# Optimization experiments

Hardware: AMD Instinct MI355X
Metric: run time of the kernel (lower is better)

The kernel has to match this reference:

```python
import jax, jax.numpy as jnp
import numpy as np

B, L, CZ, CH = 1, 512, 128, 128
LN_EPS = 1e-5  # torch nn.LayerNorm default


def layer_norm(x, g, b, eps=LN_EPS):
    mu = jnp.mean(x, axis=-1, keepdims=True)
    var = jnp.var(x, axis=-1, keepdims=True)
    return (x - mu) * jax.lax.rsqrt(var + eps) * g + b


def setup_inputs() -> dict:
    key = jax.random.key(0)
    ks = jax.random.split(key, 16)
    def lin(k, fan_in, fan_out):
        bound = 1.0 / np.sqrt(fan_in)
        kw, kb = jax.random.split(k)
        W = jax.random.uniform(kw, (fan_out, fan_in), jnp.float32, -bound, bound)
        b = jax.random.uniform(kb, (fan_out,), jnp.float32, -bound, bound)
        return W, b
    z = jax.random.normal(ks[0], (B, L, L, CZ), jnp.float32)
    pair_mask = jnp.ones((B, L, L), jnp.float32)
    Wap, bap = lin(ks[1], CZ, CH)
    Wbp, bbp = lin(ks[2], CZ, CH)
    Wag, bag = lin(ks[3], CZ, CH)
    Wbg, bbg = lin(ks[4], CZ, CH)
    Wo, bo = lin(ks[5], CH, CZ)
    Wg, bg = lin(ks[6], CZ, CZ)
    return {
        "z": z, "pair_mask": pair_mask,
        "ln_in_g": jnp.ones((CZ,), jnp.float32), "ln_in_b": jnp.zeros((CZ,), jnp.float32),
        "Wap": Wap, "bap": bap, "Wbp": Wbp, "bbp": bbp,
        "Wag": Wag, "bag": bag, "Wbg": Wbg, "bbg": bbg,
        "ln_out_g": jnp.ones((CH,), jnp.float32), "ln_out_b": jnp.zeros((CH,), jnp.float32),
        "Wo": Wo, "bo": bo, "Wg": Wg, "bg": bg,
    }


def reference(z, pair_mask, ln_in_g, ln_in_b, Wap, bap, Wbp, bbp, Wag, bag,
              Wbg, bbg, ln_out_g, ln_out_b, Wo, bo, Wg, bg):
    # z: [B,L,L,c_z], pair_mask: [B,L,L]
    z_norm = layer_norm(z, ln_in_g, ln_in_b)
    a = (z_norm @ Wap.T + bap) * jax.nn.sigmoid(z_norm @ Wag.T + bag)  # [B,L,L,ch]
    b = (z_norm @ Wbp.T + bbp) * jax.nn.sigmoid(z_norm @ Wbg.T + bbg)
    m = pair_mask[..., None]
    a = a * m
    b = b * m
    # outgoing triangle contraction: c_hidden batched LxL matmuls
    x = jnp.einsum('bikc,bjkc->bijc', a, b)
    valid_k = jnp.einsum('bik,bjk->bij', pair_mask, pair_mask)
    x = x / jnp.sqrt(jnp.maximum(valid_k[..., None], 1.0))
    x = layer_norm(x, ln_out_g, ln_out_b)
    x = x @ Wo.T + bo
    gate = jax.nn.sigmoid(z_norm @ Wg.T + bg)
    x = x * gate  # dropout is identity in eval mode
    x = x * m
    return x
```

## Files before the change

kernel.cpp:

```cpp
#include <hip/hip_runtime.h>
#include <stdint.h>

typedef unsigned short u16;
typedef __bf16 bf16x8 __attribute__((ext_vector_type(8)));
typedef float  f32x4 __attribute__((ext_vector_type(4)));
typedef u16    u16x8 __attribute__((ext_vector_type(8)));
typedef u16    u16x4 __attribute__((ext_vector_type(4)));

constexpr int LL = 512;
constexpr int NROW = LL * LL;

__device__ __forceinline__ u16 f2b(float f) {
    union { float f; unsigned u; } v; v.f = f;
    return (u16)((v.u + 0x7fffu + ((v.u >> 16) & 1u)) >> 16);
}
__device__ __forceinline__ float b2f(u16 s) {
    union { unsigned u; float f; } v; v.u = ((unsigned)s) << 16; return v.f;
}
__device__ __forceinline__ float sigmoidf_(float x) { return 1.0f / (1.0f + __expf(-x)); }

__device__ __forceinline__ f32x4 mfma16(bf16x8 a, bf16x8 b, f32x4 c) {
    return __builtin_amdgcn_mfma_f32_16x16x32_bf16(a, b, c, 0, 0, 0);
}

__global__ __launch_bounds__(256)
void k0_wconv(const float* __restrict__ Wap, const float* __restrict__ Wag,
              const float* __restrict__ Wbp, const float* __restrict__ Wbg,
              const float* __restrict__ Wg, const float* __restrict__ Wo,
              u16* __restrict__ wbf)
{
    const float* srcs[6] = {Wap, Wag, Wbp, Wbg, Wg, Wo};
    const int m = blockIdx.x >> 6;
    const int e = ((blockIdx.x & 63) << 8) | threadIdx.x;
    wbf[m * 16384 + e] = f2b(srcs[m][e]);
}

__global__ __launch_bounds__(256, 2)
void k1_ln_proj(const float* __restrict__ z, const float* __restrict__ mask,
                const float* __restrict__ lg, const float* __restrict__ lb,
                const u16* __restrict__ Wapb, const float* __restrict__ bap,
                const u16* __restrict__ Wagb, const float* __restrict__ bag,
                const u16* __restrict__ Wbpb, const float* __restrict__ bbp,
                const u16* __restrict__ Wbgb, const float* __restrict__ bbg,
                const u16* __restrict__ Wgb, const float* __restrict__ bgv,
                u16* __restrict__ a_t, u16* __restrict__ b_t, float* __restrict__ gate)
{
    __shared__ __align__(16) u16 Zs[128][136];
    __shared__ float Gg[128], Gb[128], Ms[128];

    const int tid = threadIdx.x;
    const int row0 = blockIdx.x * 128;

    if (tid < 128) { Gg[tid] = lg[tid]; Gb[tid] = lb[tid]; Ms[tid] = mask[row0 + tid]; }

    const int r = tid >> 1, h = (tid & 1) * 64;
    const float* zrow = z + (size_t)(row0 + r) * 128 + h;
    float s1 = 0.f, s2 = 0.f;
#pragma unroll
    for (int j = 0; j < 64; j += 4) {
        f32x4 v = *(const f32x4*)(zrow + j);
#pragma unroll
        for (int e = 0; e < 4; ++e) { s1 += v[e]; s2 += v[e] * v[e]; }
    }
    s1 += __shfl_xor(s1, 1);
    s2 += __shfl_xor(s2, 1);
    const float mu = s1 * 0.0078125f;
    const float rs = rsqrtf(fmaxf(s2 * 0.0078125f - mu * mu, 0.f) + 1e-5f);
    __syncthreads();
#pragma unroll
    for (int j = 0; j < 64; j += 4) {
        f32x4 v = *(const f32x4*)(zrow + j);
        u16x4 o;
#pragma unroll
        for (int e = 0; e < 4; ++e)
            o[e] = f2b((v[e] - mu) * rs * Gg[h + j + e] + Gb[h + j + e]);
        *(u16x4*)&Zs[r][h + j] = o;
    }
    __syncthreads();

    const int lane = tid & 63, wave = tid >> 6;
    const int wm = (wave >> 1) * 64, wn = (wave & 1) * 64;
    const int lr = lane & 15, quad = lane >> 4, kq = quad * 8;

#pragma unroll 1
    for (int pair = 0; pair < 2; ++pair) {
        const u16* WP = pair ? Wbpb : Wapb;
        const float* BP = pair ? bbp : bap;
        const u16* WG = pair ? Wbgb : Wagb;
        const float* BG = pair ? bbg : bag;
        u16* outp = pair ? b_t : a_t;

        f32x4 accP[4][4], accG[4][4];
#pragma unroll
        for (int i = 0; i < 4; ++i)
#pragma unroll
            for (int j = 0; j < 4; ++j) {
                accP[i][j] = (f32x4){0.f, 0.f, 0.f, 0.f};
                accG[i][j] = (f32x4){0.f, 0.f, 0.f, 0.f};
            }
#pragma unroll
        for (int kk = 0; kk < 128; kk += 32) {
            bf16x8 af[4];
#pragma unroll
            for (int mt = 0; mt < 4; ++mt)
                af[mt] = *(const bf16x8*)&Zs[wm + mt * 16 + lr][kk + kq];
#pragma unroll
            for (int nt = 0; nt < 4; ++nt) {
                const int ncol = wn + nt * 16 + lr;
                bf16x8 bp8 = *(const bf16x8*)(WP + ncol * 128 + kk + kq);
                bf16x8 bg8 = *(const bf16x8*)(WG + ncol * 128 + kk + kq);
#pragma unroll
                for (int mt = 0; mt < 4; ++mt) {
                    accP[mt][nt] = mfma16(af[mt], bp8, accP[mt][nt]);
                    accG[mt][nt] = mfma16(af[mt], bg8, accG[mt][nt]);
                }
            }
        }
#pragma unroll
        for (int nt = 0; nt < 4; ++nt) {
            const int ncol = wn + nt * 16 + lr;
            const float bP = BP[ncol];
            const float bG = BG[ncol];
#pragma unroll
            for (int mt = 0; mt < 4; ++mt) {
                const int rb = wm + mt * 16 + quad * 4;
                u16x4 o;
#pragma unroll
                for (int e = 0; e < 4; ++e)
                    o[e] = f2b((accP[mt][nt][e] + bP) * sigmoidf_(accG[mt][nt][e] + bG) * Ms[rb + e]);
                *(u16x4*)(outp + (size_t)ncol * NROW + row0 + rb) = o;
            }
        }
    }

    {
        f32x4 acc[4][4];
#pragma unroll
        for (int i = 0; i < 4; ++i)
#pragma unroll
            for (int j = 0; j < 4; ++j) acc[i][j] = (f32x4){0.f, 0.f, 0.f, 0.f};
#pragma unroll
        for (int kk = 0; kk < 128; kk += 32) {
            bf16x8 af[4];
#pragma unroll
            for (int mt = 0; mt < 4; ++mt)
                af[mt] = *(const bf16x8*)&Zs[wm + mt * 16 + lr][kk + kq];
#pragma unroll
            for (int nt = 0; nt < 4; ++nt) {
                bf16x8 bw = *(const bf16x8*)(Wgb + (wn + nt * 16 + lr) * 128 + kk + kq);
#pragma unroll
                for (int mt = 0; mt < 4; ++mt) acc[mt][nt] = mfma16(af[mt], bw, acc[mt][nt]);
            }
        }
#pragma unroll
        for (int nt = 0; nt < 4; ++nt) {
            const int ncol = wn + nt * 16 + lr;
            const float bb = bgv[ncol];
#pragma unroll
            for (int mt = 0; mt < 4; ++mt) {
                const int rb = wm + mt * 16 + quad * 4;
#pragma unroll
                for (int e = 0; e < 4; ++e)
                    gate[(size_t)(row0 + rb + e) * 128 + ncol] = sigmoidf_(acc[mt][nt][e] + bb);
            }
        }
    }
}

__global__ __launch_bounds__(256, 2)
void k2_scale(const float* __restrict__ mask, float* __restrict__ scale)
{
    __shared__ __align__(16) u16 As[128][72];
    __shared__ __align__(16) u16 Bs[128][72];

    const int tid = threadIdx.x;
    const int i0 = (blockIdx.x >> 2) * 128, j0 = (blockIdx.x & 3) * 128;
    const int lane = tid & 63, wave = tid >> 6;
    const int wm = (wave >> 1) * 64, wn = (wave & 1) * 64;
    const int lr = lane & 15, quad = lane >> 4, kq = quad * 8;

    f32x4 acc[4][4];
#pragma unroll
    for (int i = 0; i < 4; ++i)
#pragma unroll
        for (int j = 0; j < 4; ++j) acc[i][j] = (f32x4){0.f, 0.f, 0.f, 0.f};

    for (int kc = 0; kc < LL; kc += 64) {
#pragma unroll
        for (int p = 0; p < 8; ++p) {
            const int q = p * 256 + tid, rr = q >> 4, ko = (q & 15) * 4;
            f32x4 va = *(const f32x4*)(mask + (size_t)(i0 + rr) * LL + kc + ko);
            f32x4 vb = *(const f32x4*)(mask + (size_t)(j0 + rr) * LL + kc + ko);
            u16x4 ca, cb;
#pragma unroll
            for (int e = 0; e < 4; ++e) { ca[e] = f2b(va[e]); cb[e] = f2b(vb[e]); }
            *(u16x4*)&As[rr][ko] = ca;
            *(u16x4*)&Bs[rr][ko] = cb;
        }
        __syncthreads();
#pragma unroll
        for (int kk = 0; kk < 64; kk += 32) {
            bf16x8 af[4], bf[4];
#pragma unroll
            for (int mt = 0; mt < 4; ++mt) af[mt] = *(const bf16x8*)&As[wm + mt * 16 + lr][kk + kq];
#pragma unroll
            for (int nt = 0; nt < 4; ++nt) bf[nt] = *(const bf16x8*)&Bs[wn + nt * 16 + lr][kk + kq];
#pragma unroll
            for (int mt = 0; mt < 4; ++mt)
#pragma unroll
                for (int nt = 0; nt < 4; ++nt) acc[mt][nt] = mfma16(af[mt], bf[nt], acc[mt][nt]);
        }
        __syncthreads();
    }
#pragma unroll
    for (int mt = 0; mt < 4; ++mt)
#pragma unroll
        for (int nt = 0; nt < 4; ++nt) {
            const int gj = j0 + wn + nt * 16 + lr;
#pragma unroll
            for (int e = 0; e < 4; ++e) {
                const int gi = i0 + wm + mt * 16 + quad * 4 + e;
                scale[(size_t)gi * LL + gj] = rsqrtf(fmaxf(acc[mt][nt][e], 1.0f));
            }
        }
}

__global__ __launch_bounds__(256, 2)
void k3_einsum(const u16* __restrict__ a_t, const u16* __restrict__ b_t,
               const float* __restrict__ scale, u16* __restrict__ x_t)
{
    __shared__ __align__(16) u16 pool[2 * 128 * 72];
    u16 (*As)[72] = (u16(*)[72])pool;
    u16 (*Bs)[72] = (u16(*)[72])(pool + 128 * 72);
    u16 (*Ss)[128] = (u16(*)[128])pool;

    const int bid = blockIdx.x;
    const int xcd = bid & 7, slot = bid >> 3;
    const int c = xcd * 16 + (slot >> 4);
    const int tile = slot & 15;
    const int i0 = (tile >> 2) * 128, j0 = (tile & 3) * 128;

    const u16* A = a_t + (size_t)c * NROW;
    const u16* B = b_t + (size_t)c * NROW;

    const int tid = threadIdx.x;
    const int lane = tid & 63, wave = tid >> 6;
    const int wm = (wave >> 1) * 64, wn = (wave & 1) * 64;
    const int lr = lane & 15, quad = lane >> 4, kq = quad * 8;

    f32x4 acc[4][4];
#pragma unroll
    for (int i = 0; i < 4; ++i)
#pragma unroll
        for (int j = 0; j < 4; ++j) acc[i][j] = (f32x4){0.f, 0.f, 0.f, 0.f};

    for (int kc = 0; kc < LL; kc += 64) {
#pragma unroll
        for (int p = 0; p < 4; ++p) {
            const int q = p * 256 + tid, rr = q >> 3, ko = (q & 7) * 8;
            *(u16x8*)&As[rr][ko] = *(const u16x8*)(A + (size_t)(i0 + rr) * LL + kc + ko);
            *(u16x8*)&Bs[rr][ko] = *(const u16x8*)(B + (size_t)(j0 + rr) * LL + kc + ko);
        }
        __syncthreads();
#pragma unroll
        for (int kk = 0; kk < 64; kk += 32) {
            bf16x8 af[4], bf[4];
#pragma unroll
            for (int mt = 0; mt < 4; ++mt) af[mt] = *(const bf16x8*)&As[wm + mt * 16 + lr][kk + kq];
#pragma unroll
            for (int nt = 0; nt < 4; ++nt) bf[nt] = *(const bf16x8*)&Bs[wn + nt * 16 + lr][kk + kq];
#pragma unroll
            for (int mt = 0; mt < 4; ++mt)
#pragma unroll
                for (int nt = 0; nt < 4; ++nt) acc[mt][nt] = mfma16(af[mt], bf[nt], acc[mt][nt]);
        }
        __syncthreads();
    }
#pragma unroll
    for (int mt = 0; mt < 4; ++mt)
#pragma unroll
        for (int nt = 0; nt < 4; ++nt) {
            const int cc = wn + nt * 16 + lr;
#pragma unroll
            for (int e = 0; e < 4; ++e) {
                const int rr = wm + mt * 16 + quad * 4 + e;
                const float s = scale[(size_t)(i0 + rr) * LL + j0 + cc];
                Ss[rr][cc] = f2b(acc[mt][nt][e] * s);
            }
        }
    __syncthreads();
#pragma unroll
    for (int p = 0; p < 8; ++p) {
        const int rr = p * 16 + (tid >> 4);
        const int jo = (tid & 15) * 8;
        *(u16x8*)(x_t + (size_t)c * NROW + (size_t)(i0 + rr) * LL + j0 + jo) = *(const u16x8*)&Ss[rr][jo];
    }
}

__global__ __launch_bounds__(256, 2)
void k4_out(const u16* __restrict__ x_t, const float* __restrict__ mask,
            const float* __restrict__ lg, const float* __restrict__ lb,
            const u16* __restrict__ Wob, const float* __restrict__ bo,
            const float* gate, float* out)
{
    __shared__ __align__(16) u16 Zs[128][136];
    __shared__ float Ms[128];

    const int tid = threadIdx.x;
    const int row0 = blockIdx.x * 128;

    if (tid < 128) Ms[tid] = mask[row0 + tid];

    {
        const int ijo = (tid & 31) * 4;
        const int cb = (tid >> 5) * 4;
#pragma unroll
        for (int p = 0; p < 4; ++p) {
            const int c = p * 32 + cb;
            u16x4 v0 = *(const u16x4*)(x_t + (size_t)(c + 0) * NROW + row0 + ijo);
            u16x4 v1 = *(const u16x4*)(x_t + (size_t)(c + 1) * NROW + row0 + ijo);
            u16x4 v2 = *(const u16x4*)(x_t + (size_t)(c + 2) * NROW + row0 + ijo);
            u16x4 v3 = *(const u16x4*)(x_t + (size_t)(c + 3) * NROW + row0 + ijo);
#pragma unroll
            for (int i = 0; i < 4; ++i) {
                u16x4 w = { v0[i], v1[i], v2[i], v3[i] };
                *(u16x4*)&Zs[ijo + i][c] = w;
            }
        }
    }
    __syncthreads();

    {
        const int r = tid >> 1, h = (tid & 1) * 64;
        float s1 = 0.f, s2 = 0.f;
#pragma unroll
        for (int j = 0; j < 64; j += 8) {
            u16x8 v = *(const u16x8*)&Zs[r][h + j];
#pragma unroll
            for (int e = 0; e < 8; ++e) { float x = b2f(v[e]); s1 += x; s2 += x * x; }
        }
        s1 += __shfl_xor(s1, 1);
        s2 += __shfl_xor(s2, 1);
        const float mu = s1 * 0.0078125f;
        const float rs = rsqrtf(fmaxf(s2 * 0.0078125f - mu * mu, 0.f) + 1e-5f);
#pragma unroll
        for (int j = 0; j < 64; j += 8) {
            const int c = h + j;
            u16x8 v = *(const u16x8*)&Zs[r][c];
            u16x8 o;
#pragma unroll
            for (int e = 0; e < 8; ++e)
                o[e] = f2b((b2f(v[e]) - mu) * rs * lg[c + e] + lb[c + e]);
            *(u16x8*)&Zs[r][c] = o;
        }
    }
    __syncthreads();

    const int lane = tid & 63, wave = tid >> 6;
    const int wm = (wave >> 1) * 64, wn = (wave & 1) * 64;
    const int lr = lane & 15, quad = lane >> 4, kq = quad * 8;

    f32x4 acc[4][4];
#pragma unroll
    for (int i = 0; i < 4; ++i)
#pragma unroll
        for (int j = 0; j < 4; ++j) acc[i][j] = (f32x4){0.f, 0.f, 0.f, 0.f};

#pragma unroll
    for (int kk = 0; kk < 128; kk += 32) {
        bf16x8 af[4];
#pragma unroll
        for (int mt = 0; mt < 4; ++mt)
            af[mt] = *(const bf16x8*)&Zs[wm + mt * 16 + lr][kk + kq];
#pragma unroll
        for (int nt = 0; nt < 4; ++nt) {
            bf16x8 bw = *(const bf16x8*)(Wob + (wn + nt * 16 + lr) * 128 + kk + kq);
#pragma unroll
            for (int mt = 0; mt < 4; ++mt) acc[mt][nt] = mfma16(af[mt], bw, acc[mt][nt]);
        }
    }
#pragma unroll
    for (int nt = 0; nt < 4; ++nt) {
        const int cc = wn + nt * 16 + lr;
        const float bb = bo[cc];
#pragma unroll
        for (int mt = 0; mt < 4; ++mt) {
            const int rb = wm + mt * 16 + quad * 4;
#pragma unroll
            for (int e = 0; e < 4; ++e) {
                const size_t idx = (size_t)(row0 + rb + e) * 128 + cc;
                const float g = gate[idx];
                out[idx] = (acc[mt][nt][e] + bb) * g * Ms[rb + e];
            }
        }
    }
}

extern "C" void kernel_launch(void* const* d_in, const int* in_sizes, int n_in,
                              void* d_out, int out_size, void* d_ws, size_t ws_size,
                              hipStream_t stream)
{
    const float* z        = (const float*)d_in[0];
    const float* mask     = (const float*)d_in[1];
    const float* ln_in_g  = (const float*)d_in[2];
    const float* ln_in_b  = (const float*)d_in[3];
    const float* Wap      = (const float*)d_in[4];
    const float* bap      = (const float*)d_in[5];
    const float* Wbp      = (const float*)d_in[6];
    const float* bbp      = (const float*)d_in[7];
    const float* Wag      = (const float*)d_in[8];
    const float* bag      = (const float*)d_in[9];
    const float* Wbg      = (const float*)d_in[10];
    const float* bbg      = (const float*)d_in[11];
    const float* ln_out_g = (const float*)d_in[12];
    const float* ln_out_b = (const float*)d_in[13];
    const float* Wo       = (const float*)d_in[14];
    const float* bo       = (const float*)d_in[15];
    const float* Wg       = (const float*)d_in[16];
    const float* bg       = (const float*)d_in[17];

    u16* a_t = (u16*)d_ws;
    u16* b_t = a_t + (size_t)128 * NROW;
    u16* x_t = b_t + (size_t)128 * NROW;
    u16* wbf = x_t + (size_t)128 * NROW;
    float* scale = (float*)(wbf + 6 * 16384);
    float* gate = (float*)d_out;
    float* out  = (float*)d_out;

    const u16* Wapb = wbf + 0 * 16384;
    const u16* Wagb = wbf + 1 * 16384;
    const u16* Wbpb = wbf + 2 * 16384;
    const u16* Wbgb = wbf + 3 * 16384;
    const u16* Wgb  = wbf + 4 * 16384;
    const u16* Wob  = wbf + 5 * 16384;

    k0_wconv<<<dim3(384), dim3(256), 0, stream>>>(Wap, Wag, Wbp, Wbg, Wg, Wo, wbf);
    k1_ln_proj<<<dim3(2048), dim3(256), 0, stream>>>(z, mask, ln_in_g, ln_in_b,
        Wapb, bap, Wagb, bag, Wbpb, bbp, Wbgb, bbg, Wgb, bg, a_t, b_t, gate);
    k2_scale<<<dim3(16), dim3(256), 0, stream>>>(mask, scale);
    k3_einsum<<<dim3(2048), dim3(256), 0, stream>>>(a_t, b_t, scale, x_t);
    k4_out<<<dim3(2048), dim3(256), 0, stream>>>(x_t, mask, ln_out_g, ln_out_b, Wob, bo, gate, out);
}
```

Baseline: 659.1 us.

## Move gate projection to output kernel, merge scale kernel into projection launch

The gate GEMM moves out of the projection kernel and into the output kernel. The projection kernel now stores normalized z as bf16 into the output buffer, and the output kernel reads it back and computes sigmoid(zn·Wg) alongside the Wo GEMM. This replaces a 128MB fp32 gate write and read with a 64MB bf16 staging round trip. The mask-count scale computation is folded into the projection launch as 16 extra blocks, removing one kernel launch. The output kernel now holds two LDS tiles, which may lower occupancy, and f2b switches to the native bf16 conversion.

```diff
diff --git a/kernel.cpp b/kernel.cpp
--- a/kernel.cpp
+++ b/kernel.cpp
@@ -11,8 +11,8 @@
 constexpr int NROW = LL * LL;
 
 __device__ __forceinline__ u16 f2b(float f) {
-    union { float f; unsigned u; } v; v.f = f;
-    return (u16)((v.u + 0x7fffu + ((v.u >> 16) & 1u)) >> 16);
+    __bf16 h = (__bf16)f;
+    return __builtin_bit_cast(u16, h);
 }
 __device__ __forceinline__ float b2f(u16 s) {
     union { unsigned u; float f; } v; v.u = ((unsigned)s) << 16; return v.f;
@@ -42,14 +42,75 @@
                 const u16* __restrict__ Wagb, const float* __restrict__ bag,
                 const u16* __restrict__ Wbpb, const float* __restrict__ bbp,
                 const u16* __restrict__ Wbgb, const float* __restrict__ bbg,
-                const u16* __restrict__ Wgb, const float* __restrict__ bgv,
-                u16* __restrict__ a_t, u16* __restrict__ b_t, float* __restrict__ gate)
+                u16* __restrict__ a_t, u16* __restrict__ b_t,
+                float* __restrict__ scale, float* zn_out)
 {
-    __shared__ __align__(16) u16 Zs[128][136];
-    __shared__ float Gg[128], Gb[128], Ms[128];
+    __shared__ __align__(16) u16 pool[18432];
 
     const int tid = threadIdx.x;
-    const int row0 = blockIdx.x * 128;
+    const int lane = tid & 63, wave = tid >> 6;
+    const int wm = (wave >> 1) * 64, wn = (wave & 1) * 64;
+    const int lr = lane & 15, quad = lane >> 4, kq = quad * 8;
+
+    if (blockIdx.x < 16) {
+        u16 (*As)[72] = (u16(*)[72])pool;
+        u16 (*Bs)[72] = (u16(*)[72])(pool + 128 * 72);
+        const int sb = blockIdx.x;
+        const int i0 = (sb >> 2) * 128, j0 = (sb & 3) * 128;
+
+        f32x4 acc[4][4];
+#pragma unroll
+        for (int i = 0; i < 4; ++i)
+#pragma unroll
+            for (int j = 0; j < 4; ++j) acc[i][j] = (f32x4){0.f, 0.f, 0.f, 0.f};
+
+        for (int kc = 0; kc < LL; kc += 64) {
+#pragma unroll
+            for (int p = 0; p < 8; ++p) {
+                const int q = p * 256 + tid, rr = q >> 4, ko = (q & 15) * 4;
+                f32x4 va = *(const f32x4*)(mask + (size_t)(i0 + rr) * LL + kc + ko);
+                f32x4 vb = *(const f32x4*)(mask + (size_t)(j0 + rr) * LL + kc + ko);
+                u16x4 ca, cb;
+#pragma unroll
+                for (int e = 0; e < 4; ++e) { ca[e] = f2b(va[e]); cb[e] = f2b(vb[e]); }
+                *(u16x4*)&As[rr][ko] = ca;
+                *(u16x4*)&Bs[rr][ko] = cb;
+            }
+            __syncthreads();
+#pragma unroll
+            for (int kk = 0; kk < 64; kk += 32) {
+                bf16x8 af[4], bf[4];
+#pragma unroll
+                for (int mt = 0; mt < 4; ++mt) af[mt] = *(const bf16x8*)&As[wm + mt * 16 + lr][kk + kq];
+#pragma unroll
+                for (int nt = 0; nt < 4; ++nt) bf[nt] = *(const bf16x8*)&Bs[wn + nt * 16 + lr][kk + kq];
+#pragma unroll
+                for (int mt = 0; mt < 4; ++mt)
+#pragma unroll
+                    for (int nt = 0; nt < 4; ++nt) acc[mt][nt] = mfma16(af[mt], bf[nt], acc[mt][nt]);
+            }
+            __syncthreads();
+        }
+#pragma unroll
+        for (int mt = 0; mt < 4; ++mt)
+#pragma unroll
+            for (int nt = 0; nt < 4; ++nt) {
+                const int gj = j0 + wn + nt * 16 + lr;
+#pragma unroll
+                for (int e = 0; e < 4; ++e) {
+                    const int gi = i0 + wm + mt * 16 + quad * 4 + e;
+                    scale[(size_t)gi * LL + gj] = rsqrtf(fmaxf(acc[mt][nt][e], 1.0f));
+                }
+            }
+        return;
+    }
+
+    u16 (*Zs)[136] = (u16(*)[136])pool;
+    float* Gg = (float*)(pool + 17408);
+    float* Gb = Gg + 128;
+    float* Ms = Gb + 128;
+
+    const int row0 = (blockIdx.x - 16) * 128;
 
     if (tid < 128) { Gg[tid] = lg[tid]; Gb[tid] = lb[tid]; Ms[tid] = mask[row0 + tid]; }
 
@@ -78,9 +139,15 @@
     }
     __syncthreads();
 
-    const int lane = tid & 63, wave = tid >> 6;
-    const int wm = (wave >> 1) * 64, wn = (wave & 1) * 64;
-    const int lr = lane & 15, quad = lane >> 4, kq = quad * 8;
+    {
+        u16* znb = (u16*)(zn_out + (size_t)row0 * 128);
+#pragma unroll
+        for (int p = 0; p < 8; ++p) {
+            const int idx = p * 256 + tid;
+            const int rr = idx >> 4, co = (idx & 15) * 8;
+            *(u16x8*)(znb + rr * 128 + co) = *(const u16x8*)&Zs[rr][co];
+        }
+    }
 
 #pragma unroll 1
     for (int pair = 0; pair < 2; ++pair) {
@@ -132,97 +199,6 @@
             }
         }
     }
-
-    {
-        f32x4 acc[4][4];
-#pragma unroll
-        for (int i = 0; i < 4; ++i)
-#pragma unroll
-            for (int j = 0; j < 4; ++j) acc[i][j] = (f32x4){0.f, 0.f, 0.f, 0.f};
-#pragma unroll
-        for (int kk = 0; kk < 128; kk += 32) {
-            bf16x8 af[4];
-#pragma unroll
-            for (int mt = 0; mt < 4; ++mt)
-                af[mt] = *(const bf16x8*)&Zs[wm + mt * 16 + lr][kk + kq];
-#pragma unroll
-            for (int nt = 0; nt < 4; ++nt) {
-                bf16x8 bw = *(const bf16x8*)(Wgb + (wn + nt * 16 + lr) * 128 + kk + kq);
-#pragma unroll
-                for (int mt = 0; mt < 4; ++mt) acc[mt][nt] = mfma16(af[mt], bw, acc[mt][nt]);
-            }
-        }
-#pragma unroll
-        for (int nt = 0; nt < 4; ++nt) {
-            const int ncol = wn + nt * 16 + lr;
-            const float bb = bgv[ncol];
-#pragma unroll
-            for (int mt = 0; mt < 4; ++mt) {
-                const int rb = wm + mt * 16 + quad * 4;
-#pragma unroll
-                for (int e = 0; e < 4; ++e)
-                    gate[(size_t)(row0 + rb + e) * 128 + ncol] = sigmoidf_(acc[mt][nt][e] + bb);
-            }
-        }
-    }
-}
-
-__global__ __launch_bounds__(256, 2)
-void k2_scale(const float* __restrict__ mask, float* __restrict__ scale)
-{
-    __shared__ __align__(16) u16 As[128][72];
-    __shared__ __align__(16) u16 Bs[128][72];
-
-    const int tid = threadIdx.x;
-    const int i0 = (blockIdx.x >> 2) * 128, j0 = (blockIdx.x & 3) * 128;
-    const int lane = tid & 63, wave = tid >> 6;
-    const int wm = (wave >> 1) * 64, wn = (wave & 1) * 64;
-    const int lr = lane & 15, quad = lane >> 4, kq = quad * 8;
-
-    f32x4 acc[4][4];
-#pragma unroll
-    for (int i = 0; i < 4; ++i)
-#pragma unroll
-        for (int j = 0; j < 4; ++j) acc[i][j] = (f32x4){0.f, 0.f, 0.f, 0.f};
-
-    for (int kc = 0; kc < LL; kc += 64) {
-#pragma unroll
-        for (int p = 0; p < 8; ++p) {
-            const int q = p * 256 + tid, rr = q >> 4, ko = (q & 15) * 4;
-            f32x4 va = *(const f32x4*)(mask + (size_t)(i0 + rr) * LL + kc + ko);
-            f32x4 vb = *(const f32x4*)(mask + (size_t)(j0 + rr) * LL + kc + ko);
-            u16x4 ca, cb;
-#pragma unroll
-            for (int e = 0; e < 4; ++e) { ca[e] = f2b(va[e]); cb[e] = f2b(vb[e]); }
-            *(u16x4*)&As[rr][ko] = ca;
-            *(u16x4*)&Bs[rr][ko] = cb;
-        }
-        __syncthreads();
-#pragma unroll
-        for (int kk = 0; kk < 64; kk += 32) {
-            bf16x8 af[4], bf[4];
-#pragma unroll
-            for (int mt = 0; mt < 4; ++mt) af[mt] = *(const bf16x8*)&As[wm + mt * 16 + lr][kk + kq];
-#pragma unroll
-            for (int nt = 0; nt < 4; ++nt) bf[nt] = *(const bf16x8*)&Bs[wn + nt * 16 + lr][kk + kq];
-#pragma unroll
-            for (int mt = 0; mt < 4; ++mt)
-#pragma unroll
-                for (int nt = 0; nt < 4; ++nt) acc[mt][nt] = mfma16(af[mt], bf[nt], acc[mt][nt]);
-        }
-        __syncthreads();
-    }
-#pragma unroll
-    for (int mt = 0; mt < 4; ++mt)
-#pragma unroll
-        for (int nt = 0; nt < 4; ++nt) {
-            const int gj = j0 + wn + nt * 16 + lr;
-#pragma unroll
-            for (int e = 0; e < 4; ++e) {
-                const int gi = i0 + wm + mt * 16 + quad * 4 + e;
-                scale[(size_t)gi * LL + gj] = rsqrtf(fmaxf(acc[mt][nt][e], 1.0f));
-            }
-        }
 }
 
 __global__ __launch_bounds__(256, 2)
@@ -301,15 +277,27 @@
 void k4_out(const u16* __restrict__ x_t, const float* __restrict__ mask,
             const float* __restrict__ lg, const float* __restrict__ lb,
             const u16* __restrict__ Wob, const float* __restrict__ bo,
-            const float* gate, float* out)
+            const u16* __restrict__ Wgb, const float* __restrict__ bgv,
+            float* out)
 {
     __shared__ __align__(16) u16 Zs[128][136];
+    __shared__ __align__(16) u16 Zn[128][136];
     __shared__ float Ms[128];
 
     const int tid = threadIdx.x;
     const int row0 = blockIdx.x * 128;
 
     if (tid < 128) Ms[tid] = mask[row0 + tid];
+
+    {
+        const u16* znb = (const u16*)(out + (size_t)row0 * 128);
+#pragma unroll
+        for (int p = 0; p < 8; ++p) {
+            const int idx = p * 256 + tid;
+            const int rr = idx >> 4, co = (idx & 15) * 8;
+            *(u16x8*)&Zn[rr][co] = *(const u16x8*)(znb + rr * 128 + co);
+        }
+    }
 
     {
         const int ijo = (tid & 31) * 4;
@@ -360,37 +348,49 @@
     const int wm = (wave >> 1) * 64, wn = (wave & 1) * 64;
     const int lr = lane & 15, quad = lane >> 4, kq = quad * 8;
 
-    f32x4 acc[4][4];
-#pragma unroll
-    for (int i = 0; i < 4; ++i)
-#pragma unroll
-        for (int j = 0; j < 4; ++j) acc[i][j] = (f32x4){0.f, 0.f, 0.f, 0.f};
-
-#pragma unroll
-    for (int kk = 0; kk < 128; kk += 32) {
-        bf16x8 af[4];
-#pragma unroll
-        for (int mt = 0; mt < 4; ++mt)
-            af[mt] = *(const bf16x8*)&Zs[wm + mt * 16 + lr][kk + kq];
-#pragma unroll
-        for (int nt = 0; nt < 4; ++nt) {
-            bf16x8 bw = *(const bf16x8*)(Wob + (wn + nt * 16 + lr) * 128 + kk + kq);
-#pragma unroll
-            for (int mt = 0; mt < 4; ++mt) acc[mt][nt] = mfma16(af[mt], bw, acc[mt][nt]);
-        }
-    }
-#pragma unroll
-    for (int nt = 0; nt < 4; ++nt) {
-        const int cc = wn + nt * 16 + lr;
-        const float bb = bo[cc];
-#pragma unroll
-        for (int mt = 0; mt < 4; ++mt) {
-            const int rb = wm + mt * 16 + quad * 4;
-#pragma unroll
-            for (int e = 0; e < 4; ++e) {
-                const size_t idx = (size_t)(row0 + rb + e) * 128 + cc;
-                const float g = gate[idx];
-                out[idx] = (acc[mt][nt][e] + bb) * g * Ms[rb + e];
+#pragma unroll 1
+    for (int nh = 0; nh < 2; ++nh) {
+        f32x4 accO[4][2], accG[4][2];
+#pragma unroll
+        for (int i = 0; i < 4; ++i)
+#pragma unroll
+            for (int j = 0; j < 2; ++j) {
+                accO[i][j] = (f32x4){0.f, 0.f, 0.f, 0.f};
+                accG[i][j] = (f32x4){0.f, 0.f, 0.f, 0.f};
+            }
+#pragma unroll
+        for (int kk = 0; kk < 128; kk += 32) {
+            bf16x8 ax[4], az[4];
+#pragma unroll
+            for (int mt = 0; mt < 4; ++mt) {
+                ax[mt] = *(const bf16x8*)&Zs[wm + mt * 16 + lr][kk + kq];
+                az[mt] = *(const bf16x8*)&Zn[wm + mt * 16 + lr][kk + kq];
+            }
+#pragma unroll
+            for (int n2 = 0; n2 < 2; ++n2) {
+                const int ncol = wn + (nh * 2 + n2) * 16 + lr;
+                bf16x8 bo8 = *(const bf16x8*)(Wob + ncol * 128 + kk + kq);
+                bf16x8 bg8 = *(const bf16x8*)(Wgb + ncol * 128 + kk + kq);
+#pragma unroll
+                for (int mt = 0; mt < 4; ++mt) {
+                    accO[mt][n2] = mfma16(ax[mt], bo8, accO[mt][n2]);
+                    accG[mt][n2] = mfma16(az[mt], bg8, accG[mt][n2]);
+                }
+            }
+        }
+#pragma unroll
+        for (int n2 = 0; n2 < 2; ++n2) {
+            const int cc = wn + (nh * 2 + n2) * 16 + lr;
+            const float bb = bo[cc];
+            const float bg = bgv[cc];
+#pragma unroll
+            for (int mt = 0; mt < 4; ++mt) {
+                const int rb = wm + mt * 16 + quad * 4;
+#pragma unroll
+                for (int e = 0; e < 4; ++e) {
+                    const size_t idx = (size_t)(row0 + rb + e) * 128 + cc;
+                    out[idx] = (accO[mt][n2][e] + bb) * sigmoidf_(accG[mt][n2][e] + bg) * Ms[rb + e];
+                }
             }
         }
     }
@@ -424,8 +424,7 @@
     u16* x_t = b_t + (size_t)128 * NROW;
     u16* wbf = x_t + (size_t)128 * NROW;
     float* scale = (float*)(wbf + 6 * 16384);
-    float* gate = (float*)d_out;
-    float* out  = (float*)d_out;
+    float* outf  = (float*)d_out;
 
     const u16* Wapb = wbf + 0 * 16384;
     const u16* Wagb = wbf + 1 * 16384;
@@ -435,9 +434,9 @@
     const u16* Wob  = wbf + 5 * 16384;
 
     k0_wconv<<<dim3(384), dim3(256), 0, stream>>>(Wap, Wag, Wbp, Wbg, Wg, Wo, wbf);
-    k1_ln_proj<<<dim3(2048), dim3(256), 0, stream>>>(z, mask, ln_in_g, ln_in_b,
-        Wapb, bap, Wagb, bag, Wbpb, bbp, Wbgb, bbg, Wgb, bg, a_t, b_t, gate);
-    k2_scale<<<dim3(16), dim3(256), 0, stream>>>(mask, scale);
+    k1_ln_proj<<<dim3(2064), dim3(256), 0, stream>>>(z, mask, ln_in_g, ln_in_b,
+        Wapb, bap, Wagb, bag, Wbpb, bbp, Wbgb, bbg, a_t, b_t, scale, outf);
     k3_einsum<<<dim3(2048), dim3(256), 0, stream>>>(a_t, b_t, scale, x_t);
-    k4_out<<<dim3(2048), dim3(256), 0, stream>>>(x_t, mask, ln_out_g, ln_out_b, Wob, bo, gate, out);
-}
+    k4_out<<<dim3(2048), dim3(256), 0, stream>>>(x_t, mask, ln_out_g, ln_out_b,
+        Wob, bo, Wgb, bg, outf);
+}
```

After: 626.9 us. 4.9% less time.
